# Kernel optimization log

Measured on AMD Instinct MI355X. Metric: run time of the kernel, lower is better.

## Reference

```python
import jax, jax.numpy as jnp
import numpy as np

N = 20000        # nodes
E = 640000       # edges (avg degree 32)
D_IN = 128       # node_features
D_HID = 256      # conv_booster * D_IN
D_DENSE = 128    # D_HID // linear_decay
N_CLASSES = 2


def _glorot(key, fan_in, fan_out):
    s = np.sqrt(1.0 / fan_in).astype(np.float32)
    return jax.random.normal(key, (fan_in, fan_out), jnp.float32) * s


def setup_inputs() -> dict:
    key = jax.random.key(0)
    ks = jax.random.split(key, 12)
    return {
        "node_features": jax.random.normal(ks[0], (N, D_IN), jnp.float32),
        "edge_index": jax.random.randint(ks[1], (2, E), 0, N, dtype=jnp.int32),
        "edge_weight": jax.random.uniform(ks[2], (E,), jnp.float32),
        "W1": _glorot(ks[3], D_IN, D_HID),
        "b1": jnp.zeros((D_HID,), jnp.float32),
        "W2": _glorot(ks[4], D_HID, D_HID),
        "b2": jnp.zeros((D_HID,), jnp.float32),
        "Wd1": _glorot(ks[5], D_HID, D_DENSE),
        "bd1": jnp.zeros((D_DENSE,), jnp.float32),
        "Wd2": _glorot(ks[6], D_DENSE, N_CLASSES),
        "bd2": jnp.zeros((N_CLASSES,), jnp.float32),
    }


def gcn_conv(x, row, col, w, W, b, n):
    # PyG GCNConv: add self-loops (weight 1), symmetric normalization,
    # x' = D^{-1/2}(A+I)D^{-1/2} (x W) + b
    h = x @ W                                        # [n, out]
    loop = jnp.arange(n, dtype=row.dtype)
    r = jnp.concatenate([row, loop])
    c = jnp.concatenate([col, loop])
    ww = jnp.concatenate([w, jnp.ones((n,), w.dtype)])
    deg = jax.ops.segment_sum(ww, c, num_segments=n)  # degree at targets
    dinv = jnp.where(deg > 0, jax.lax.rsqrt(deg), 0.0)
    norm = dinv[r] * ww * dinv[c]                    # [E+n]
    msg = norm[:, None] * h[r]                       # gather + scale (hot path)
    return jax.ops.segment_sum(msg, c, num_segments=n) + b  # scatter-add


def reference(node_features, edge_index, edge_weight,
              W1, b1, W2, b2, Wd1, bd1, Wd2, bd2):
    row, col = edge_index[0], edge_index[1]
    n = node_features.shape[0]
    h = gcn_conv(node_features, row, col, edge_weight, W1, b1, n)
    h = gcn_conv(h, row, col, edge_weight, W2, b2, n)
    g = jnp.mean(h, axis=0)                          # MeanAggregation pooling
    z = jax.nn.relu(g @ Wd1 + bd1)
    logits = z @ Wd2 + bd2
    return jax.nn.softmax(logits)
```

## Files before the change

kernel.cpp:

```cpp
#include <hip/hip_runtime.h>
#include <hip/hip_bf16.h>


#define D_IN 128
#define D_HID 256
#define D_DENSE 128
#define R0 10240
#define NSL 128
#define NFOLD 250
#define FOLD_C 80
#define NTILE 157

__global__ __launch_bounds__(1024) void k_scatter(
    const int* __restrict__ tgt, const int* __restrict__ src,
    const float* __restrict__ w, const float* __restrict__ dinv,
    const float* __restrict__ u, float* __restrict__ part,
    unsigned* __restrict__ ctr, int E, int N, int mode) {
    __shared__ float acc[R0];
    if (mode == 0 && blockIdx.x == 0 && threadIdx.x == 0) ctr[0] = 0u;
    const int range = blockIdx.x & 1;
    const int slice = blockIdx.x >> 1;
    const int base  = range ? R0 : 0;
    const int lim   = range ? (N - R0) : R0;
    const int per = (E + NSL - 1) / NSL;
    const int e0 = slice * per, e1 = min(e0 + per, E);
    float* outp = part + (range ? (size_t)NSL * R0 + (size_t)slice * lim
                                : (size_t)slice * lim);
    for (int i = threadIdx.x; i < lim; i += 1024) acc[i] = 0.f;
    __syncthreads();
    for (int e = e0 + threadIdx.x; e < e1; e += 1024) {
        int t = tgt[e] - base;
        if ((unsigned)t < (unsigned)lim) {
            float v = w[e];
            if (mode != 0) {
                int c = src[e];
                float dc = dinv[c];
                v *= (mode == 2) ? dc * u[c] : dc;
            }
            atomicAdd(&acc[t], v);
        }
    }
    __syncthreads();
    for (int i = threadIdx.x; i < lim; i += 1024) outp[i] = acc[i];
}

__global__ __launch_bounds__(1024) void k_fold(
    const float* __restrict__ part, float* __restrict__ dinv,
    float* __restrict__ u, float* __restrict__ S_u_part,
    const float* __restrict__ W1, const float* __restrict__ b1,
    const float* __restrict__ W2, float* __restrict__ M, float* __restrict__ c2,
    int N, int mode) {
    __shared__ float lds[1044];
    const int b = blockIdx.x, tid = threadIdx.x;

    if (b >= NFOLD) {
        int q = b - NFOLD;
        lds[tid] = W2[(tid >> 2) * 256 + q * 4 + (tid & 3)];
        __syncthreads();
        int wvi = tid >> 6, lane = tid & 63;
        for (int kr = 0; kr < 8; ++kr) {
            int k = wvi * 8 + kr;
            float a0 = 0, a1 = 0, a2 = 0, a3 = 0;
            #pragma unroll
            for (int it = 0; it < 4; ++it) {
                int j = it * 64 + lane;
                float a = W1[k * 256 + j];
                a0 += a * lds[j*4+0]; a1 += a * lds[j*4+1];
                a2 += a * lds[j*4+2]; a3 += a * lds[j*4+3];
            }
            #pragma unroll
            for (int off = 32; off > 0; off >>= 1) {
                a0 += __shfl_down(a0, off, 64); a1 += __shfl_down(a1, off, 64);
                a2 += __shfl_down(a2, off, 64); a3 += __shfl_down(a3, off, 64);
            }
            if (lane == 0) {
                M[k * 256 + q*4 + 0] = a0; M[k * 256 + q*4 + 1] = a1;
                M[k * 256 + q*4 + 2] = a2; M[k * 256 + q*4 + 3] = a3;
            }
        }
        if (wvi == 0) {
            float a0 = 0, a1 = 0, a2 = 0, a3 = 0;
            #pragma unroll
            for (int it = 0; it < 4; ++it) {
                int j = it * 64 + lane;
                float a = b1[j];
                a0 += a * lds[j*4+0]; a1 += a * lds[j*4+1];
                a2 += a * lds[j*4+2]; a3 += a * lds[j*4+3];
            }
            #pragma unroll
            for (int off = 32; off > 0; off >>= 1) {
                a0 += __shfl_down(a0, off, 64); a1 += __shfl_down(a1, off, 64);
                a2 += __shfl_down(a2, off, 64); a3 += __shfl_down(a3, off, 64);
            }
            if (lane == 0) {
                c2[q*4+0] = a0; c2[q*4+1] = a1;
                c2[q*4+2] = a2; c2[q*4+3] = a3;
            }
        }
        return;
    }

    const int j = tid & 127, rg = tid >> 7;
    const int i = b * FOLD_C + j;
    const bool act = (j < FOLD_C) && (i < N);
    float sv = 0.f;
    if (act) {
        size_t st; const float* pp;
        if (i < R0) { st = R0;               pp = part + i; }
        else        { st = (size_t)(N - R0); pp = part + (size_t)NSL * R0 + (i - R0); }
        pp += (size_t)rg * 16 * st;
        #pragma unroll
        for (int r = 0; r < 16; ++r) sv += pp[(size_t)r * st];
    }
    lds[rg * 128 + j] = sv;
    __syncthreads();
    float ui = 0.f;
    if (rg == 0) {
        float tot = 0.f;
        #pragma unroll
        for (int q = 0; q < 8; ++q) tot += lds[q * 128 + j];
        if (act) {
            if (mode == 0) dinv[i] = rsqrtf(tot + 1.0f);
            else { float d = dinv[i]; ui = d * (tot + d); u[i] = ui; }
        }
    }
    if (mode == 1) {
        float v = ui;
        #pragma unroll
        for (int off = 32; off > 0; off >>= 1) v += __shfl_down(v, off, 64);
        if ((tid & 63) == 0) lds[1028 + (tid >> 6)] = v;
        __syncthreads();
        if (tid == 0) {
            float t2 = 0.f;
            #pragma unroll
            for (int q = 0; q < 16; ++q) t2 += lds[1028 + q];
            S_u_part[b] = t2;
        }
    }
}

__device__ __forceinline__ void g_arrive(unsigned* ctr) {
    __syncthreads();
    if (threadIdx.x == 0)
        __hip_atomic_fetch_add(ctr, 1u, __ATOMIC_RELEASE, __HIP_MEMORY_SCOPE_AGENT);
}
__device__ __forceinline__ void g_wait(unsigned* ctr, unsigned target) {
    if (threadIdx.x == 0) {
        while (__hip_atomic_load(ctr, __ATOMIC_ACQUIRE, __HIP_MEMORY_SCOPE_AGENT) < target)
            __builtin_amdgcn_s_sleep(2);
    }
    __syncthreads();
}

__global__ __launch_bounds__(1024) void k_tail(
    const float* __restrict__ x, const float* __restrict__ part,
    const float* __restrict__ dinv, const float* __restrict__ u,
    const float* __restrict__ S_u_part, const float* __restrict__ M,
    const float* __restrict__ c2, const float* __restrict__ b2,
    const float* __restrict__ Wd1, const float* __restrict__ bd1,
    const float* __restrict__ Wd2, const float* __restrict__ bd2,
    float* __restrict__ s_part, float* __restrict__ g_part,
    float* __restrict__ z_part, float* __restrict__ S_u_g,
    unsigned* __restrict__ ctr, float* __restrict__ out,
    int N, float inv_n) {
    __shared__ float sh[1024];
    __shared__ float wvl[128];
    __shared__ float ss[128];
    __shared__ float gv[16];
    __shared__ float su[16];
    const int b = blockIdx.x, tid = threadIdx.x;
    const int k = tid & 127, rg = tid >> 7;

    if (b < NTILE) {
        const int i0 = b * 128;
        const int i = i0 + k;
        const bool act = i < N;
        float sv = 0.f;
        if (act) {
            size_t st; const float* pp;
            if (i < R0) { st = R0;               pp = part + i; }
            else        { st = (size_t)(N - R0); pp = part + (size_t)NSL * R0 + (i - R0); }
            pp += (size_t)rg * 16 * st;
            #pragma unroll
            for (int r = 0; r < 16; ++r) sv += pp[(size_t)r * st];
        }
        sh[tid] = sv;
        __syncthreads();
        if (rg == 0) {
            float q = 0.f;
            #pragma unroll
            for (int t2 = 0; t2 < 8; ++t2) q += sh[t2 * 128 + k];
            float d = act ? dinv[i] : 0.f;
            wvl[k] = act ? d * (q + d * u[i]) : 0.f;
        }
        __syncthreads();
        float acc = 0.f;
        #pragma unroll
        for (int jj = 0; jj < 16; ++jj) {
            int m = rg + 8 * jj;
            int i2 = i0 + m;
            float xv = x[(size_t)(i2 < N ? i2 : i0) * D_IN + k];
            acc += wvl[m] * xv;
        }
        sh[tid] = acc;
        __syncthreads();
        if (rg == 0) {
            float t2s = 0.f;
            #pragma unroll
            for (int t2 = 0; t2 < 8; ++t2) t2s += sh[t2 * 128 + k];
            s_part[b * 128 + k] = t2s;
        }
    }
    g_arrive(ctr);
    if (b >= 16) return;
    g_wait(ctr, 256);

    {
        float a2 = 0.f;
        for (int q = rg; q < NTILE; q += 8) a2 += s_part[q * 128 + k];
        sh[tid] = a2;
        float v = 0.f;
        if (b == 0) {
            v = (tid < NFOLD) ? S_u_part[tid] : 0.f;
            #pragma unroll
            for (int off = 32; off > 0; off >>= 1) v += __shfl_down(v, off, 64);
        }
        __syncthreads();
        if (rg == 0) {
            float t2 = 0.f;
            #pragma unroll
            for (int q = 0; q < 8; ++q) t2 += sh[q * 128 + k];
            ss[k] = t2;
        }
        if (b == 0 && (tid & 63) == 0) su[tid >> 6] = v;
        __syncthreads();
        if (b == 0 && tid == 0) {
            float t2 = 0.f;
            #pragma unroll
            for (int q = 0; q < 16; ++q) t2 += su[q];
            S_u_g[0] = t2;
        }
        if (tid < 256) {
            float gp = 0.f;
            #pragma unroll
            for (int kk = 0; kk < 8; ++kk)
                gp += ss[b * 8 + kk] * M[(b * 8 + kk) * 256 + tid];
            g_part[b * 256 + tid] = gp;
        }
    }
    g_arrive(ctr);
    g_wait(ctr, 272);

    {
        if (tid < 16) {
            int kk = b * 16 + tid;
            float gval = 0.f;
            #pragma unroll
            for (int p2 = 0; p2 < 16; ++p2) gval += g_part[p2 * 256 + kk];
            gv[tid] = (gval + S_u_g[0] * c2[kk]) * inv_n + b2[kk];
        }
        __syncthreads();
        if (tid < 128) {
            float z = 0.f;
            #pragma unroll
            for (int kk = 0; kk < 16; ++kk)
                z += gv[kk] * Wd1[(b * 16 + kk) * D_DENSE + tid];
            z_part[b * 128 + tid] = z;
        }
    }
    g_arrive(ctr);
    if (b != 0) return;
    g_wait(ctr, 288);

    float p0 = 0.f, p1 = 0.f;
    if (tid < 128) {
        float zr = bd1[tid];
        #pragma unroll
        for (int p2 = 0; p2 < 16; ++p2) zr += z_part[p2 * 128 + tid];
        float zt = fmaxf(zr, 0.f);
        p0 = zt * Wd2[tid * 2 + 0];
        p1 = zt * Wd2[tid * 2 + 1];
    }
    #pragma unroll
    for (int off = 32; off > 0; off >>= 1) {
        p0 += __shfl_down(p0, off, 64);
        p1 += __shfl_down(p1, off, 64);
    }
    if ((tid & 63) == 0) { sh[tid >> 6] = p0; sh[32 + (tid >> 6)] = p1; }
    __syncthreads();
    if (tid == 0) {
        float l0 = bd2[0], l1 = bd2[1];
        #pragma unroll
        for (int q = 0; q < 16; ++q) { l0 += sh[q]; l1 += sh[32 + q]; }
        float m = fmaxf(l0, l1);
        float e0 = expf(l0 - m), e1 = expf(l1 - m);
        float inv = 1.0f / (e0 + e1);
        out[0] = e0 * inv;
        out[1] = e1 * inv;
    }
}

extern "C" void kernel_launch(void* const* d_in, const int* in_sizes, int n_in,
                              void* d_out, int out_size, void* d_ws, size_t ws_size,
                              hipStream_t stream) {
    const float* x   = (const float*)d_in[0];
    const int*   ei  = (const int*)  d_in[1];
    const float* w   = (const float*)d_in[2];
    const float* W1  = (const float*)d_in[3];
    const float* b1  = (const float*)d_in[4];
    const float* W2  = (const float*)d_in[5];
    const float* b2  = (const float*)d_in[6];
    const float* Wd1 = (const float*)d_in[7];
    const float* bd1 = (const float*)d_in[8];
    const float* Wd2 = (const float*)d_in[9];
    const float* bd2 = (const float*)d_in[10];
    float* out = (float*)d_out;

    const int N = in_sizes[0] / D_IN;
    const int E = in_sizes[1] / 2;
    const int* row = ei;
    const int* col = ei + E;

    unsigned* ctr = (unsigned*)d_ws;
    float* fws    = (float*)d_ws + 16;
    float* part   = fws;
    float* dinv   = part + (size_t)NSL * N;
    float* u      = dinv + N;
    float* s_part = u + N;
    float* S_u_p  = s_part + (size_t)NTILE * D_IN;
    float* S_u_g  = S_u_p + NFOLD;
    float* M      = S_u_g + 1;
    float* c2     = M + D_IN * D_HID;
    float* g_part = c2 + D_HID;
    float* z_part = g_part + 16 * D_HID;

    k_scatter<<<2 * NSL, 1024, 0, stream>>>(col, row, w, dinv, u, part, ctr, E, N, 0);
    k_fold<<<NFOLD + 64, 1024, 0, stream>>>(part, dinv, u, S_u_p, W1, b1, W2, M, c2, N, 0);
    k_scatter<<<2 * NSL, 1024, 0, stream>>>(row, col, w, dinv, u, part, ctr, E, N, 1);
    k_fold<<<NFOLD, 1024, 0, stream>>>(part, dinv, u, S_u_p, W1, b1, W2, M, c2, N, 1);
    k_scatter<<<2 * NSL, 1024, 0, stream>>>(row, col, w, dinv, u, part, ctr, E, N, 2);
    k_tail<<<256, 1024, 0, stream>>>(x, part, dinv, u, S_u_p, M, c2, b2,
                                     Wd1, bd1, Wd2, bd2, s_part, g_part, z_part,
                                     S_u_g, ctr, out, N, 1.0f / (float)N);
}
```

Measured before the change: 150.6 us.

## Fuse all scatter/fold/tail phases into one persistent kernel with grid barriers

Replaces the six separate kernel launches (three scatters, two folds, tail) with a single persistent 256-block kernel that separates phases with atomic-counter grid barriers. The W1·W2 fold is overlapped with the first barrier wait. Fold work is re-tiled to 157 blocks of 128 nodes. The intent is to remove launch gaps and per-kernel ramp-up. In exchange, correctness depends on all 256 blocks being co-resident, and each block now carries the 40KB LDS accumulator through every phase.

Result: slower. 255.5 us (+69.6%).

```diff
diff --git a/kernel.cpp b/kernel.cpp
--- a/kernel.cpp
+++ b/kernel.cpp
@@ -1,5 +1,4 @@
 #include <hip/hip_runtime.h>
-#include <hip/hip_bf16.h>
 
 
 #define D_IN 128
@@ -7,28 +6,39 @@
 #define D_DENSE 128
 #define R0 10240
 #define NSL 128
-#define NFOLD 250
-#define FOLD_C 80
 #define NTILE 157
-
-__global__ __launch_bounds__(1024) void k_scatter(
-    const int* __restrict__ tgt, const int* __restrict__ src,
+#define MBASE NTILE
+
+__device__ __forceinline__ void g_arrive(unsigned* ctr) {
+    __syncthreads();
+    if (threadIdx.x == 0)
+        __hip_atomic_fetch_add(ctr, 1u, __ATOMIC_RELEASE, __HIP_MEMORY_SCOPE_AGENT);
+}
+__device__ __forceinline__ void g_wait(unsigned* ctr, unsigned target) {
+    if (threadIdx.x == 0) {
+        while (__hip_atomic_load(ctr, __ATOMIC_ACQUIRE, __HIP_MEMORY_SCOPE_AGENT) < target)
+            __builtin_amdgcn_s_sleep(2);
+    }
+    __syncthreads();
+}
+
+__device__ __forceinline__ void scatter_phase(
+    float* acc, const int* __restrict__ tgt, const int* __restrict__ src,
     const float* __restrict__ w, const float* __restrict__ dinv,
     const float* __restrict__ u, float* __restrict__ part,
-    unsigned* __restrict__ ctr, int E, int N, int mode) {
-    __shared__ float acc[R0];
-    if (mode == 0 && blockIdx.x == 0 && threadIdx.x == 0) ctr[0] = 0u;
-    const int range = blockIdx.x & 1;
-    const int slice = blockIdx.x >> 1;
+    int E, int N, int mode, int b, int tid)
+{
+    const int range = b & 1;
+    const int slice = b >> 1;
     const int base  = range ? R0 : 0;
     const int lim   = range ? (N - R0) : R0;
     const int per = (E + NSL - 1) / NSL;
     const int e0 = slice * per, e1 = min(e0 + per, E);
     float* outp = part + (range ? (size_t)NSL * R0 + (size_t)slice * lim
                                 : (size_t)slice * lim);
-    for (int i = threadIdx.x; i < lim; i += 1024) acc[i] = 0.f;
-    __syncthreads();
-    for (int e = e0 + threadIdx.x; e < e1; e += 1024) {
+    for (int i = tid; i < lim; i += 1024) acc[i] = 0.f;
+    __syncthreads();
+    for (int e = e0 + tid; e < e1; e += 1024) {
         int t = tgt[e] - base;
         if ((unsigned)t < (unsigned)lim) {
             float v = w[e];
@@ -41,68 +51,13 @@
         }
     }
     __syncthreads();
-    for (int i = threadIdx.x; i < lim; i += 1024) outp[i] = acc[i];
-}
-
-__global__ __launch_bounds__(1024) void k_fold(
-    const float* __restrict__ part, float* __restrict__ dinv,
-    float* __restrict__ u, float* __restrict__ S_u_part,
-    const float* __restrict__ W1, const float* __restrict__ b1,
-    const float* __restrict__ W2, float* __restrict__ M, float* __restrict__ c2,
-    int N, int mode) {
-    __shared__ float lds[1044];
-    const int b = blockIdx.x, tid = threadIdx.x;
-
-    if (b >= NFOLD) {
-        int q = b - NFOLD;
-        lds[tid] = W2[(tid >> 2) * 256 + q * 4 + (tid & 3)];
-        __syncthreads();
-        int wvi = tid >> 6, lane = tid & 63;
-        for (int kr = 0; kr < 8; ++kr) {
-            int k = wvi * 8 + kr;
-            float a0 = 0, a1 = 0, a2 = 0, a3 = 0;
-            #pragma unroll
-            for (int it = 0; it < 4; ++it) {
-                int j = it * 64 + lane;
-                float a = W1[k * 256 + j];
-                a0 += a * lds[j*4+0]; a1 += a * lds[j*4+1];
-                a2 += a * lds[j*4+2]; a3 += a * lds[j*4+3];
-            }
-            #pragma unroll
-            for (int off = 32; off > 0; off >>= 1) {
-                a0 += __shfl_down(a0, off, 64); a1 += __shfl_down(a1, off, 64);
-                a2 += __shfl_down(a2, off, 64); a3 += __shfl_down(a3, off, 64);
-            }
-            if (lane == 0) {
-                M[k * 256 + q*4 + 0] = a0; M[k * 256 + q*4 + 1] = a1;
-                M[k * 256 + q*4 + 2] = a2; M[k * 256 + q*4 + 3] = a3;
-            }
-        }
-        if (wvi == 0) {
-            float a0 = 0, a1 = 0, a2 = 0, a3 = 0;
-            #pragma unroll
-            for (int it = 0; it < 4; ++it) {
-                int j = it * 64 + lane;
-                float a = b1[j];
-                a0 += a * lds[j*4+0]; a1 += a * lds[j*4+1];
-                a2 += a * lds[j*4+2]; a3 += a * lds[j*4+3];
-            }
-            #pragma unroll
-            for (int off = 32; off > 0; off >>= 1) {
-                a0 += __shfl_down(a0, off, 64); a1 += __shfl_down(a1, off, 64);
-                a2 += __shfl_down(a2, off, 64); a3 += __shfl_down(a3, off, 64);
-            }
-            if (lane == 0) {
-                c2[q*4+0] = a0; c2[q*4+1] = a1;
-                c2[q*4+2] = a2; c2[q*4+3] = a3;
-            }
-        }
-        return;
-    }
-
-    const int j = tid & 127, rg = tid >> 7;
-    const int i = b * FOLD_C + j;
-    const bool act = (j < FOLD_C) && (i < N);
+    for (int i = tid; i < lim; i += 1024) outp[i] = acc[i];
+}
+
+__device__ __forceinline__ float fold_tot(
+    const float* __restrict__ part, float* sh,
+    int i, bool act, int rg, int tid, int k, int N)
+{
     float sv = 0.f;
     if (act) {
         size_t st; const float* pp;
@@ -112,57 +67,31 @@
         #pragma unroll
         for (int r = 0; r < 16; ++r) sv += pp[(size_t)r * st];
     }
-    lds[rg * 128 + j] = sv;
-    __syncthreads();
-    float ui = 0.f;
+    sh[tid] = sv;
+    __syncthreads();
+    float tot = 0.f;
     if (rg == 0) {
-        float tot = 0.f;
-        #pragma unroll
-        for (int q = 0; q < 8; ++q) tot += lds[q * 128 + j];
-        if (act) {
-            if (mode == 0) dinv[i] = rsqrtf(tot + 1.0f);
-            else { float d = dinv[i]; ui = d * (tot + d); u[i] = ui; }
-        }
-    }
-    if (mode == 1) {
-        float v = ui;
-        #pragma unroll
-        for (int off = 32; off > 0; off >>= 1) v += __shfl_down(v, off, 64);
-        if ((tid & 63) == 0) lds[1028 + (tid >> 6)] = v;
-        __syncthreads();
-        if (tid == 0) {
-            float t2 = 0.f;
-            #pragma unroll
-            for (int q = 0; q < 16; ++q) t2 += lds[1028 + q];
-            S_u_part[b] = t2;
-        }
-    }
-}
-
-__device__ __forceinline__ void g_arrive(unsigned* ctr) {
-    __syncthreads();
-    if (threadIdx.x == 0)
-        __hip_atomic_fetch_add(ctr, 1u, __ATOMIC_RELEASE, __HIP_MEMORY_SCOPE_AGENT);
-}
-__device__ __forceinline__ void g_wait(unsigned* ctr, unsigned target) {
-    if (threadIdx.x == 0) {
-        while (__hip_atomic_load(ctr, __ATOMIC_ACQUIRE, __HIP_MEMORY_SCOPE_AGENT) < target)
-            __builtin_amdgcn_s_sleep(2);
-    }
-    __syncthreads();
-}
-
-__global__ __launch_bounds__(1024) void k_tail(
-    const float* __restrict__ x, const float* __restrict__ part,
-    const float* __restrict__ dinv, const float* __restrict__ u,
-    const float* __restrict__ S_u_part, const float* __restrict__ M,
-    const float* __restrict__ c2, const float* __restrict__ b2,
+        #pragma unroll
+        for (int q = 0; q < 8; ++q) tot += sh[q * 128 + k];
+    }
+    return tot;
+}
+
+__global__ __launch_bounds__(1024) void k_mega(
+    const float* __restrict__ x, const int* __restrict__ row,
+    const int* __restrict__ col, const float* __restrict__ w,
+    const float* __restrict__ W1, const float* __restrict__ b1,
+    const float* __restrict__ W2, const float* __restrict__ b2,
     const float* __restrict__ Wd1, const float* __restrict__ bd1,
     const float* __restrict__ Wd2, const float* __restrict__ bd2,
-    float* __restrict__ s_part, float* __restrict__ g_part,
-    float* __restrict__ z_part, float* __restrict__ S_u_g,
+    float* __restrict__ part, float* __restrict__ dinv, float* __restrict__ u,
+    float* __restrict__ s_part, float* __restrict__ S_u_part,
+    float* __restrict__ S_u_g, float* __restrict__ M, float* __restrict__ c2,
+    float* __restrict__ g_part, float* __restrict__ z_part,
     unsigned* __restrict__ ctr, float* __restrict__ out,
-    int N, float inv_n) {
+    int N, int E, float inv_n)
+{
+    __shared__ float acc[R0];
     __shared__ float sh[1024];
     __shared__ float wvl[128];
     __shared__ float ss[128];
@@ -171,38 +100,107 @@
     const int b = blockIdx.x, tid = threadIdx.x;
     const int k = tid & 127, rg = tid >> 7;
 
+    scatter_phase(acc, col, row, w, dinv, u, part, E, N, 0, b, tid);
+    g_arrive(ctr);
+
+    if (b >= MBASE && b < MBASE + 64) {
+        const int q = b - MBASE;
+        sh[tid] = W2[(tid >> 2) * 256 + q * 4 + (tid & 3)];
+        __syncthreads();
+        const int wvi = tid >> 6, lane = tid & 63;
+        for (int kr = 0; kr < 8; ++kr) {
+            int kk = wvi * 8 + kr;
+            float a0 = 0, a1 = 0, a2 = 0, a3 = 0;
+            #pragma unroll
+            for (int it = 0; it < 4; ++it) {
+                int j = it * 64 + lane;
+                float a = W1[kk * 256 + j];
+                a0 += a * sh[j*4+0]; a1 += a * sh[j*4+1];
+                a2 += a * sh[j*4+2]; a3 += a * sh[j*4+3];
+            }
+            #pragma unroll
+            for (int off = 32; off > 0; off >>= 1) {
+                a0 += __shfl_down(a0, off, 64); a1 += __shfl_down(a1, off, 64);
+                a2 += __shfl_down(a2, off, 64); a3 += __shfl_down(a3, off, 64);
+            }
+            if (lane == 0) {
+                M[kk * 256 + q*4 + 0] = a0; M[kk * 256 + q*4 + 1] = a1;
+                M[kk * 256 + q*4 + 2] = a2; M[kk * 256 + q*4 + 3] = a3;
+            }
+        }
+        if (wvi == 0) {
+            float a0 = 0, a1 = 0, a2 = 0, a3 = 0;
+            #pragma unroll
+            for (int it = 0; it < 4; ++it) {
+                int j = it * 64 + lane;
+                float a = b1[j];
+                a0 += a * sh[j*4+0]; a1 += a * sh[j*4+1];
+                a2 += a * sh[j*4+2]; a3 += a * sh[j*4+3];
+            }
+            #pragma unroll
+            for (int off = 32; off > 0; off >>= 1) {
+                a0 += __shfl_down(a0, off, 64); a1 += __shfl_down(a1, off, 64);
+                a2 += __shfl_down(a2, off, 64); a3 += __shfl_down(a3, off, 64);
+            }
+            if (lane == 0) {
+                c2[q*4+0] = a0; c2[q*4+1] = a1;
+                c2[q*4+2] = a2; c2[q*4+3] = a3;
+            }
+        }
+    }
+    g_wait(ctr, 256);
+
+    if (b < NTILE) {
+        const int i = b * 128 + k;
+        const bool act = i < N;
+        float tot = fold_tot(part, sh, i, act, rg, tid, k, N);
+        if (rg == 0 && act) dinv[i] = rsqrtf(tot + 1.0f);
+    }
+    g_arrive(ctr); g_wait(ctr, 512);
+
+    scatter_phase(acc, row, col, w, dinv, u, part, E, N, 1, b, tid);
+    g_arrive(ctr); g_wait(ctr, 768);
+
+    if (b < NTILE) {
+        const int i = b * 128 + k;
+        const bool act = i < N;
+        float tot = fold_tot(part, sh, i, act, rg, tid, k, N);
+        float ui = 0.f;
+        if (rg == 0 && act) { float d = dinv[i]; ui = d * (tot + d); u[i] = ui; }
+        __syncthreads();
+        if (rg == 0) {
+            float v = ui;
+            #pragma unroll
+            for (int off = 32; off > 0; off >>= 1) v += __shfl_down(v, off, 64);
+            if ((tid & 63) == 0) sh[tid >> 6] = v;
+        }
+        __syncthreads();
+        if (tid == 0) S_u_part[b] = sh[0] + sh[1];
+    }
+    g_arrive(ctr); g_wait(ctr, 1024);
+
+    scatter_phase(acc, row, col, w, dinv, u, part, E, N, 2, b, tid);
+    g_arrive(ctr); g_wait(ctr, 1280);
+
     if (b < NTILE) {
         const int i0 = b * 128;
         const int i = i0 + k;
         const bool act = i < N;
-        float sv = 0.f;
-        if (act) {
-            size_t st; const float* pp;
-            if (i < R0) { st = R0;               pp = part + i; }
-            else        { st = (size_t)(N - R0); pp = part + (size_t)NSL * R0 + (i - R0); }
-            pp += (size_t)rg * 16 * st;
-            #pragma unroll
-            for (int r = 0; r < 16; ++r) sv += pp[(size_t)r * st];
-        }
-        sh[tid] = sv;
-        __syncthreads();
+        float tot = fold_tot(part, sh, i, act, rg, tid, k, N);
         if (rg == 0) {
-            float q = 0.f;
-            #pragma unroll
-            for (int t2 = 0; t2 < 8; ++t2) q += sh[t2 * 128 + k];
             float d = act ? dinv[i] : 0.f;
-            wvl[k] = act ? d * (q + d * u[i]) : 0.f;
-        }
-        __syncthreads();
-        float acc = 0.f;
+            wvl[k] = act ? d * (tot + d * u[i]) : 0.f;
+        }
+        __syncthreads();
+        float a = 0.f;
         #pragma unroll
         for (int jj = 0; jj < 16; ++jj) {
             int m = rg + 8 * jj;
             int i2 = i0 + m;
             float xv = x[(size_t)(i2 < N ? i2 : i0) * D_IN + k];
-            acc += wvl[m] * xv;
-        }
-        sh[tid] = acc;
+            a += wvl[m] * xv;
+        }
+        sh[tid] = a;
         __syncthreads();
         if (rg == 0) {
             float t2s = 0.f;
@@ -213,7 +211,7 @@
     }
     g_arrive(ctr);
     if (b >= 16) return;
-    g_wait(ctr, 256);
+    g_wait(ctr, 1536);
 
     {
         float a2 = 0.f;
@@ -221,7 +219,7 @@
         sh[tid] = a2;
         float v = 0.f;
         if (b == 0) {
-            v = (tid < NFOLD) ? S_u_part[tid] : 0.f;
+            v = (tid < NTILE) ? S_u_part[tid] : 0.f;
             #pragma unroll
             for (int off = 32; off > 0; off >>= 1) v += __shfl_down(v, off, 64);
         }
@@ -248,8 +246,7 @@
             g_part[b * 256 + tid] = gp;
         }
     }
-    g_arrive(ctr);
-    g_wait(ctr, 272);
+    g_arrive(ctr); g_wait(ctr, 1552);
 
     {
         if (tid < 16) {
@@ -270,7 +267,7 @@
     }
     g_arrive(ctr);
     if (b != 0) return;
-    g_wait(ctr, 288);
+    g_wait(ctr, 1568);
 
     float p0 = 0.f, p1 = 0.f;
     if (tid < 128) {
@@ -328,18 +325,16 @@
     float* u      = dinv + N;
     float* s_part = u + N;
     float* S_u_p  = s_part + (size_t)NTILE * D_IN;
-    float* S_u_g  = S_u_p + NFOLD;
+    float* S_u_g  = S_u_p + NTILE;
     float* M      = S_u_g + 1;
     float* c2     = M + D_IN * D_HID;
     float* g_part = c2 + D_HID;
     float* z_part = g_part + 16 * D_HID;
 
-    k_scatter<<<2 * NSL, 1024, 0, stream>>>(col, row, w, dinv, u, part, ctr, E, N, 0);
-    k_fold<<<NFOLD + 64, 1024, 0, stream>>>(part, dinv, u, S_u_p, W1, b1, W2, M, c2, N, 0);
-    k_scatter<<<2 * NSL, 1024, 0, stream>>>(row, col, w, dinv, u, part, ctr, E, N, 1);
-    k_fold<<<NFOLD, 1024, 0, stream>>>(part, dinv, u, S_u_p, W1, b1, W2, M, c2, N, 1);
-    k_scatter<<<2 * NSL, 1024, 0, stream>>>(row, col, w, dinv, u, part, ctr, E, N, 2);
-    k_tail<<<256, 1024, 0, stream>>>(x, part, dinv, u, S_u_p, M, c2, b2,
-                                     Wd1, bd1, Wd2, bd2, s_part, g_part, z_part,
-                                     S_u_g, ctr, out, N, 1.0f / (float)N);
-}
+    hipMemsetAsync(ctr, 0, 16 * sizeof(unsigned), stream);
+    k_mega<<<256, 1024, 0, stream>>>(x, row, col, w, W1, b1, W2, b2,
+                                     Wd1, bd1, Wd2, bd2,
+                                     part, dinv, u, s_part, S_u_p, S_u_g,
+                                     M, c2, g_part, z_part, ctr, out,
+                                     N, E, 1.0f / (float)N);
+}
```
